# Optimization experiments

Measured on AMD Instinct MI355X. Metric: run time of the kernel, lower is better.

## Reference

```python
import jax, jax.numpy as jnp
import numpy as np

EPS = 1e-8


def setup_inputs() -> dict:
    key = jax.random.key(0)
    ks = jax.random.split(key, 5)
    B, C, F, T = 2, 8, 1024, 256
    Ch, Fh = 4 * C, 4 * F  # expanded channels/features
    s_pw1 = 1.0 / np.sqrt(F)
    s_dw1 = 1.0 / np.sqrt(C)
    s_pw2 = 1.0 / np.sqrt(Fh)
    s_dw2 = 1.0 / np.sqrt(Ch)
    return {
        "x": jax.random.normal(ks[0], (B, C, F, T), jnp.float32),
        "ln_w": jnp.ones((C, F), jnp.float32),
        "ln_b": jnp.zeros((C, F), jnp.float32),
        "pw1": jax.random.uniform(ks[1], (C, Fh, F), jnp.float32, -s_pw1, s_pw1),
        "dw1": jax.random.uniform(ks[2], (Ch, C), jnp.float32, -s_dw1, s_dw1),
        "pw2": jax.random.uniform(ks[3], (Ch, F, Fh), jnp.float32, -s_pw2, s_pw2),
        "dw2": jax.random.uniform(ks[4], (C, Ch), jnp.float32, -s_dw2, s_dw2),
    }


def _mc_layernorm(x, w, b):
    # x: (B,C,F,T); normalize over feature axis (2), affine per (channel, feature)
    mu = jnp.mean(x, axis=2, keepdims=True)
    var = jnp.var(x, axis=2, keepdims=True)
    xn = (x - mu) * jax.lax.rsqrt(var + EPS)
    return xn * w[None, :, :, None] + b[None, :, :, None]


def reference(x, ln_w, ln_b, pw1, dw1, pw2, dw2):
    h = _mc_layernorm(x, ln_w, ln_b)
    # per-channel positionwise linear: (C, F_out, F_in)
    h = jnp.einsum('bcft,cgf->bcgt', h, pw1)
    # channel mixing (depthwise linear across channels): (C_out, C_in)
    h = jnp.einsum('bcft,dc->bdft', h, dw1)
    h = jnp.square(jax.nn.relu(h))  # squared ReLU
    h = jnp.einsum('bcft,cgf->bcgt', h, pw2)
    h = jnp.einsum('bcft,dc->bdft', h, dw2)
    return x + h
```

## Files before the change

kernel.cpp:

```cpp
#include <hip/hip_runtime.h>

#define B_DIM  2
#define C_DIM  8
#define F_DIM  1024
#define T_DIM  256
#define CH_DIM 32
#define FH_DIM 4096
#define BT_DIM 512

typedef __bf16 bf16x8 __attribute__((ext_vector_type(8)));
typedef __bf16 bf16x4 __attribute__((ext_vector_type(4)));
typedef float  f32x4  __attribute__((ext_vector_type(4)));

__device__ __forceinline__ void async16(const void* g, void* l) {
  __builtin_amdgcn_global_load_lds(
      (const __attribute__((address_space(1))) unsigned int*)g,
      (__attribute__((address_space(3))) unsigned int*)l, 16, 0, 0);
}

#define LGKM0_SCHED() do { \
    asm volatile("s_waitcnt lgkmcnt(0)" ::: "memory"); \
    __builtin_amdgcn_sched_barrier(0); } while (0)

__global__ void ln_kernel(const float* __restrict__ x,
                          const float* __restrict__ lnw,
                          const float* __restrict__ lnb,
                          __bf16* __restrict__ hn) {
  const int tb = blockIdx.x;
  const int c  = blockIdx.y;
  const int b  = blockIdx.z;
  const int tid = threadIdx.x;
  const int t0 = tb * 16;

  extern __shared__ __align__(16) float xs[];
  __shared__ float ps[16][64], ps2[16][64];
  __shared__ float mean_s[16], rstd_s[16];

  const float* xp = x + (size_t)(b * C_DIM + c) * F_DIM * T_DIM;

  const int fbase = tid >> 2;
  const int tq    = tid & 3;

  float s0 = 0.f, s1 = 0.f, s2v = 0.f, s3 = 0.f;
  float q0 = 0.f, q1 = 0.f, q2 = 0.f, q3 = 0.f;
#pragma unroll 4
  for (int it = 0; it < 16; ++it) {
    const int f = it * 64 + fbase;
    const float4 v = *(const float4*)(xp + (size_t)f * T_DIM + t0 + tq * 4);
    xs[(tq * 4 + 0) * 1028 + f] = v.x;
    xs[(tq * 4 + 1) * 1028 + f] = v.y;
    xs[(tq * 4 + 2) * 1028 + f] = v.z;
    xs[(tq * 4 + 3) * 1028 + f] = v.w;
    s0 += v.x; q0 += v.x * v.x;
    s1 += v.y; q1 += v.y * v.y;
    s2v += v.z; q2 += v.z * v.z;
    s3 += v.w; q3 += v.w * v.w;
  }
  ps[tq * 4 + 0][fbase] = s0;  ps2[tq * 4 + 0][fbase] = q0;
  ps[tq * 4 + 1][fbase] = s1;  ps2[tq * 4 + 1][fbase] = q1;
  ps[tq * 4 + 2][fbase] = s2v; ps2[tq * 4 + 2][fbase] = q2;
  ps[tq * 4 + 3][fbase] = s3;  ps2[tq * 4 + 3][fbase] = q3;
  __syncthreads();
  if (tid < 16) {
    float a = 0.f, a2 = 0.f;
    for (int j = 0; j < 64; ++j) { a += ps[tid][j]; a2 += ps2[tid][j]; }
    const float mu  = a * (1.0f / F_DIM);
    const float var = a2 * (1.0f / F_DIM) - mu * mu;
    mean_s[tid] = mu;
    rstd_s[tid] = rsqrtf(var + 1e-8f);
  }
  __syncthreads();

  const int wv = tid >> 6, lane = tid & 63;
  const float* lw = lnw + c * F_DIM;
  const float* lb = lnb + c * F_DIM;
#pragma unroll
  for (int p = 0; p < 4; ++p) {
    const int t = wv * 4 + p;
    const float mu = mean_s[t], rs = rstd_s[t];
    __bf16* hp = hn + ((size_t)c * BT_DIM + b * T_DIM + t0 + t) * F_DIM;
#pragma unroll
    for (int j = 0; j < 8; ++j) {
      const int f = j * 128 + lane * 2;
      const float a = xs[t * 1028 + f];
      const float bb = xs[t * 1028 + f + 1];
      const float r0 = (a - mu) * rs * lw[f] + lb[f];
      const float r1 = (bb - mu) * rs * lw[f + 1] + lb[f + 1];
      __bf16 o2[2] = { (__bf16)r0, (__bf16)r1 };
      *(ushort*)nullptr == *(ushort*)nullptr;
      *(uint*)(hp + f) = *(uint*)o2;
    }
  }
}

template<int TPB_BITS, bool CT>
__global__ __launch_bounds__(512, 2)
void gemm_4p(const float* __restrict__ A, const __bf16* __restrict__ Bm,
             __bf16* __restrict__ Co, const int M, const int K) {
  const int NT = K >> 6;
  const int bid = blockIdx.x;
  const int xcd = bid & 7, idx = bid >> 3;
  const int batch = xcd * (32 >> TPB_BITS) + (idx >> TPB_BITS);
  const int tile  = idx & ((1 << TPB_BITS) - 1);
  const int mt = tile >> 1, nt = tile & 1;

  const int tid = threadIdx.x, lane = tid & 63, wid = tid >> 6;

  const float*  Ab = A  + (size_t)batch * M * K + (size_t)(mt * 256) * K;
  const __bf16* Bb = Bm + (size_t)batch * BT_DIM * K + (size_t)(nt * 256) * K;

  extern __shared__ __align__(16) char smem[];
  __bf16* const AS = (__bf16*)smem;
  __bf16* const BS = (__bf16*)(smem + 65536);

  const int wm = wid >> 2, wn = wid & 3;
  const int lr = lane & 15, khi = lane >> 4;
  const int lsw = lr & 7;

  const int b_row = lane >> 3;
  const int b_src = (lane & 7) ^ b_row;

  f32x4 acc[8][4] = {};
  float4 sa[8];
  bf16x8 af[4];

  auto issueB1 = [&](int sbuf, int tt, int j) {
    const int chunk = j * 8 + wid;
    async16(Bb + (size_t)(chunk * 8 + b_row) * K + (size_t)tt * 64 + b_src * 8,
            BS + sbuf * 16384 + chunk * 512);
  };
  auto issueA2 = [&](int tt, int i0) {
#pragma unroll
    for (int i = i0; i < i0 + 2; ++i) {
      const int c = i * 512 + tid;
      sa[i] = *(const float4*)(Ab + (size_t)(c >> 4) * K + (size_t)tt * 64 + (c & 15) * 4);
    }
  };
  auto writeA2 = [&](int abuf, int i0) {
#pragma unroll
    for (int i = i0; i < i0 + 2; ++i) {
      const int c = i * 512 + tid;
      const int r = c >> 4;
      const int s = ((c & 15) >> 1) ^ (r & 7);
      bf16x4 v;
      v[0]=(__bf16)sa[i].x; v[1]=(__bf16)sa[i].y; v[2]=(__bf16)sa[i].z; v[3]=(__bf16)sa[i].w;
      *(bf16x4*)(AS + abuf * 16384 + r * 64 + s * 8 + (c & 1) * 4) = v;
    }
  };
  auto readA = [&](int abuf, int mq, int ks) {
#pragma unroll
    for (int j = 0; j < 4; ++j) {
      const int row = wm * 128 + (mq * 4 + j) * 16 + lr;
      af[j] = *(const bf16x8*)(AS + abuf * 16384 + row * 64 + (((ks << 2) | khi) ^ lsw) * 8);
    }
  };
  auto readB4 = [&](bf16x8* bq, int rbuf, int ks) {
#pragma unroll
    for (int ni = 0; ni < 4; ++ni) {
      const int row = wn * 64 + ni * 16 + lr;
      bq[ni] = *(const bf16x8*)(BS + rbuf * 16384 + row * 64 + (((ks << 2) | khi) ^ lsw) * 8);
    }
  };
  auto mfma16 = [&](const bf16x8* bq, int mq) {
    __builtin_amdgcn_s_setprio(1);
#pragma unroll
    for (int j = 0; j < 4; ++j)
#pragma unroll
      for (int n = 0; n < 4; ++n)
        acc[mq * 4 + j][n] =
            __builtin_amdgcn_mfma_f32_16x16x32_bf16(af[j], bq[n], acc[mq * 4 + j][n], 0, 0, 0);
    __builtin_amdgcn_s_setprio(0);
  };

  issueA2(0, 0); issueA2(0, 2); issueA2(0, 4); issueA2(0, 6);
  issueB1(0, 0, 0); issueB1(0, 0, 1); issueB1(0, 0, 2); issueB1(0, 0, 3);
  issueB1(1, 1, 0); issueB1(1, 1, 1); issueB1(1, 1, 2); issueB1(1, 1, 3);
  writeA2(0, 0); writeA2(0, 2); writeA2(0, 4); writeA2(0, 6);
  issueA2(1, 0); issueA2(1, 2); issueA2(1, 4); issueA2(1, 6);
  asm volatile("s_waitcnt vmcnt(12)" ::: "memory");
  LGKM0_SCHED();
  __builtin_amdgcn_s_barrier();

  int cur = 0;
  for (int t = 0; t < NT; ++t) {
    const int rd = t % 3, st = (t + 2) % 3;
    const int tN = (t + 2 < NT) ? t + 2 : NT - 1;
    bf16x8 bq[4];
    issueB1(st, tN, 0); issueB1(st, tN, 1);
    readA(cur, 0, 0); readB4(bq, rd, 0);
    __builtin_amdgcn_s_barrier(); LGKM0_SCHED();
    mfma16(bq, 0); __builtin_amdgcn_s_barrier();
    issueB1(st, tN, 2); issueB1(st, tN, 3);
    readA(cur, 1, 0);
    __builtin_amdgcn_s_barrier(); LGKM0_SCHED();
    mfma16(bq, 1); __builtin_amdgcn_s_barrier();
    writeA2(cur ^ 1, 0); issueA2(tN, 0);
    writeA2(cur ^ 1, 2); issueA2(tN, 2);
    readA(cur, 0, 1); readB4(bq, rd, 1);
    __builtin_amdgcn_s_barrier(); LGKM0_SCHED();
    mfma16(bq, 0); __builtin_amdgcn_s_barrier();
    writeA2(cur ^ 1, 4); issueA2(tN, 4);
    writeA2(cur ^ 1, 6); issueA2(tN, 6);
    readA(cur, 1, 1);
    __builtin_amdgcn_s_barrier(); LGKM0_SCHED();
    mfma16(bq, 1);
    __builtin_amdgcn_s_barrier();
    cur ^= 1;
  }

  const int colc = lane & 15;
  const int rowb = (lane >> 4) * 4;
  if (CT) {
    __bf16* T = (__bf16*)smem + wid * 1152;
#pragma unroll
    for (int h = 0; h < 2; ++h) {
      const int mbase = mt * 256 + wm * 128 + h * 64;
#pragma unroll
      for (int ni = 0; ni < 4; ++ni) {
#pragma unroll
        for (int mi = 0; mi < 4; ++mi)
#pragma unroll
          for (int r = 0; r < 4; ++r)
            T[colc * 72 + mi * 16 + rowb + r] = (__bf16)acc[h * 4 + mi][ni][r];
        __bf16* outp = Co + (size_t)batch * BT_DIM * M
                          + (size_t)(nt * 256 + wn * 64 + ni * 16) * M + mbase + lane;
#pragma unroll
        for (int r16 = 0; r16 < 16; ++r16)
          outp[(size_t)r16 * M] = T[r16 * 72 + lane];
      }
    }
  } else {
#pragma unroll
    for (int mi = 0; mi < 8; ++mi) {
#pragma unroll
      for (int ni = 0; ni < 4; ++ni) {
        const int m = mt * 256 + wm * 128 + mi * 16 + rowb;
        const int n = nt * 256 + wn * 64 + ni * 16 + colc;
#pragma unroll
        for (int r = 0; r < 4; ++r)
          Co[((size_t)batch * M + m + r) * BT_DIM + n] = (__bf16)acc[mi][ni][r];
      }
    }
  }
}

__global__ void mix1_kernel(const __bf16* __restrict__ Y1,
                            const float* __restrict__ dw1,
                            __bf16* __restrict__ h2) {
  const int gidx = blockIdx.x * 256 + threadIdx.x;
  const int g8 = gidx & 511, bt = gidx >> 9;
  const int g0 = g8 * 8;

  float y[C_DIM][8];
#pragma unroll
  for (int c = 0; c < C_DIM; ++c) {
    bf16x8 v = *(const bf16x8*)(Y1 + ((size_t)c * BT_DIM + bt) * FH_DIM + g0);
#pragma unroll
    for (int j = 0; j < 8; ++j) y[c][j] = (float)v[j];
  }
  for (int d = 0; d < CH_DIM; ++d) {
    float s[8] = {0.f,0.f,0.f,0.f,0.f,0.f,0.f,0.f};
#pragma unroll
    for (int c = 0; c < C_DIM; ++c) {
      const float wv = dw1[d * C_DIM + c];
#pragma unroll
      for (int j = 0; j < 8; ++j) s[j] += wv * y[c][j];
    }
    bf16x8 o;
#pragma unroll
    for (int j = 0; j < 8; ++j) {
      float r = s[j] > 0.f ? s[j] : 0.f;
      o[j] = (__bf16)(r * r);
    }
    *(bf16x8*)(h2 + ((size_t)d * BT_DIM + bt) * FH_DIM + g0) = o;
  }
}

__global__ void mix2_kernel(const float* __restrict__ x,
                            const __bf16* __restrict__ Y2,
                            const float* __restrict__ dw2,
                            float* __restrict__ out) {
  const int gidx = blockIdx.x * 256 + threadIdx.x;
  const int t4 = gidx & 63;
  const int f  = (gidx >> 6) & 1023;
  const int b  = gidx >> 16;
  const int t0 = t4 * 4;

  float4 r[C_DIM];
#pragma unroll
  for (int dd = 0; dd < C_DIM; ++dd)
    r[dd] = *(const float4*)(x + ((size_t)(b * C_DIM + dd) * F_DIM + f) * T_DIM + t0);

  for (int d = 0; d < CH_DIM; ++d) {
    bf16x4 v = *(const bf16x4*)(Y2 + ((size_t)d * F_DIM + f) * BT_DIM + b * T_DIM + t0);
    const float v0 = (float)v[0], v1 = (float)v[1], v2 = (float)v[2], v3 = (float)v[3];
#pragma unroll
    for (int dd = 0; dd < C_DIM; ++dd) {
      const float w = dw2[dd * CH_DIM + d];
      r[dd].x += w * v0; r[dd].y += w * v1; r[dd].z += w * v2; r[dd].w += w * v3;
    }
  }
#pragma unroll
  for (int dd = 0; dd < C_DIM; ++dd)
    *(float4*)(out + ((size_t)(b * C_DIM + dd) * F_DIM + f) * T_DIM + t0) = r[dd];
}

extern "C" void kernel_launch(void* const* d_in, const int* in_sizes, int n_in,
                              void* d_out, int out_size, void* d_ws, size_t ws_size,
                              hipStream_t stream) {
  const float* x   = (const float*)d_in[0];
  const float* lnw = (const float*)d_in[1];
  const float* lnb = (const float*)d_in[2];
  const float* pw1 = (const float*)d_in[3];
  const float* dw1 = (const float*)d_in[4];
  const float* pw2 = (const float*)d_in[5];
  const float* dw2 = (const float*)d_in[6];
  float* out = (float*)d_out;

  char* ws = (char*)d_ws;
  __bf16* hn = (__bf16*)(ws);
  __bf16* Y1 = (__bf16*)(ws + (8ULL << 20));
  __bf16* h2 = (__bf16*)(ws + (40ULL << 20));
  __bf16* Y2 = (__bf16*)(ws);

  (void)hipFuncSetAttribute((const void*)ln_kernel,
                            hipFuncAttributeMaxDynamicSharedMemorySize, 65792);
  (void)hipFuncSetAttribute((const void*)gemm_4p<5, true>,
                            hipFuncAttributeMaxDynamicSharedMemorySize, 163840);
  (void)hipFuncSetAttribute((const void*)gemm_4p<3, false>,
                            hipFuncAttributeMaxDynamicSharedMemorySize, 163840);

  ln_kernel<<<dim3(T_DIM / 16, C_DIM, B_DIM), 256, 65792, stream>>>(x, lnw, lnb, hn);
  gemm_4p<5, true><<<256, 512, 163840, stream>>>(pw1, hn, Y1, FH_DIM, F_DIM);
  mix1_kernel<<<(BT_DIM * (FH_DIM / 8)) / 256, 256, 0, stream>>>(Y1, dw1, h2);
  gemm_4p<3, false><<<256, 512, 163840, stream>>>(pw2, h2, Y2, F_DIM, FH_DIM);
  mix2_kernel<<<512, 256, 0, stream>>>(x, Y2, dw2, out);
}
```

Before: 293.7 us.

## Replace pw2 GEMM with smaller-tile double-buffered kernel using more blocks

Replaces the second per-channel GEMM (pw2 over K=4096) with a dedicated kernel that uses 128x128 tiles, 256 threads, static double-buffered LDS and register-staged fp32-to-bf16 conversion of A. It launches 1024 blocks instead of 256 so more CUs get work and several blocks can be resident per CU. The cost is smaller tiles, which means less reuse per loaded byte and more A traffic. It also removes a stray null-pointer comparison statement in the layernorm kernel.

```diff
diff --git a/kernel.cpp b/kernel.cpp
--- a/kernel.cpp
+++ b/kernel.cpp
@@ -87,7 +87,6 @@
       const float r0 = (a - mu) * rs * lw[f] + lb[f];
       const float r1 = (bb - mu) * rs * lw[f + 1] + lb[f + 1];
       __bf16 o2[2] = { (__bf16)r0, (__bf16)r1 };
-      *(ushort*)nullptr == *(ushort*)nullptr;
       *(uint*)(hp + f) = *(uint*)o2;
     }
   }
@@ -244,6 +243,111 @@
   }
 }
 
+__global__ __launch_bounds__(256, 3)
+void gemm_pw2(const float* __restrict__ A, const __bf16* __restrict__ Bm,
+              __bf16* __restrict__ Co) {
+  const int M = F_DIM, K = FH_DIM;
+  const int bid = blockIdx.x;
+  const int xcd = bid & 7, idx = bid >> 3;
+  const int q   = idx & 31;
+  const int nt  = idx >> 5;
+  const int batch = xcd * 4 + (q >> 3);
+  const int mt    = q & 7;
+
+  const int tid = threadIdx.x, lane = tid & 63, wid = tid >> 6;
+
+  const float*  Ab = A  + (size_t)batch * M * K + (size_t)(mt * 128) * K;
+  const __bf16* Bb = Bm + (size_t)batch * BT_DIM * K + (size_t)(nt * 128) * K;
+
+  __shared__ __align__(16) __bf16 As[2][128 * 32];
+  __shared__ __align__(16) __bf16 Bs[2][128 * 32];
+
+  const int a_r  = tid >> 3;
+  const int a_c8 = tid & 7;
+
+  const int wm = (wid >> 1) * 64, wn = (wid & 1) * 64;
+  const int lr = lane & 15, khi = lane >> 4;
+  const int lswz = (lr >> 1) & 3;
+
+  f32x4 acc[4][4] = {};
+  float4 sa[4];
+  const int NT = K >> 5;
+
+  auto issueA = [&](int tt) {
+#pragma unroll
+    for (int i = 0; i < 4; ++i)
+      sa[i] = *(const float4*)(Ab + (size_t)(a_r + 32 * i) * K + tt * 32 + a_c8 * 4);
+  };
+  auto writeA = [&](int buf) {
+#pragma unroll
+    for (int i = 0; i < 4; ++i) {
+      const int row = a_r + 32 * i;
+      bf16x4 v;
+      v[0] = (__bf16)sa[i].x; v[1] = (__bf16)sa[i].y;
+      v[2] = (__bf16)sa[i].z; v[3] = (__bf16)sa[i].w;
+      const int slot = (a_c8 >> 1) ^ ((row >> 1) & 3);
+      *(bf16x4*)(&As[buf][row * 32 + slot * 8 + (a_c8 & 1) * 4]) = v;
+    }
+  };
+  auto issueB = [&](int buf, int tt) {
+#pragma unroll
+    for (int j = 0; j < 2; ++j) {
+      const int chunk = wid * 2 + j;
+      const int r = chunk * 16 + (lane >> 2);
+      const int s = (lane & 3) ^ ((r >> 1) & 3);
+      async16(Bb + (size_t)r * K + (size_t)tt * 32 + s * 8,
+              &Bs[buf][chunk * 512]);
+    }
+  };
+  auto compute = [&](int buf) {
+    bf16x8 af[4], bq[4];
+    const int soff = (khi ^ lswz) * 8;
+#pragma unroll
+    for (int mi = 0; mi < 4; ++mi)
+      af[mi] = *(const bf16x8*)(&As[buf][(wm + mi * 16 + lr) * 32 + soff]);
+#pragma unroll
+    for (int ni = 0; ni < 4; ++ni)
+      bq[ni] = *(const bf16x8*)(&Bs[buf][(wn + ni * 16 + lr) * 32 + soff]);
+    __builtin_amdgcn_s_setprio(1);
+#pragma unroll
+    for (int mi = 0; mi < 4; ++mi)
+#pragma unroll
+      for (int ni = 0; ni < 4; ++ni)
+        acc[mi][ni] = __builtin_amdgcn_mfma_f32_16x16x32_bf16(af[mi], bq[ni], acc[mi][ni], 0, 0, 0);
+    __builtin_amdgcn_s_setprio(0);
+  };
+
+  issueA(0);
+  issueB(0, 0);
+  writeA(0);
+  __syncthreads();
+
+  int buf = 0;
+  for (int t = 0; t < NT; ++t) {
+    const int tn = (t + 1 < NT) ? t + 1 : t;
+    issueA(tn);
+    issueB(buf ^ 1, tn);
+    compute(buf);
+    writeA(buf ^ 1);
+    __syncthreads();
+    buf ^= 1;
+  }
+
+  const int colc = lane & 15;
+  const int rowb = (lane >> 4) * 4;
+#pragma unroll
+  for (int mi = 0; mi < 4; ++mi) {
+#pragma unroll
+    for (int ni = 0; ni < 4; ++ni) {
+      const int m = mt * 128 + wm + mi * 16 + rowb;
+      const int n = nt * 128 + wn + ni * 16 + colc;
+#pragma unroll
+      for (int r = 0; r < 4; ++r)
+        Co[((size_t)batch * M + m + r) * BT_DIM + n] = (__bf16)acc[mi][ni][r];
+    }
+  }
+}
+
 __global__ void mix1_kernel(const __bf16* __restrict__ Y1,
                             const float* __restrict__ dw1,
                             __bf16* __restrict__ h2) {
@@ -327,12 +431,10 @@
                             hipFuncAttributeMaxDynamicSharedMemorySize, 65792);
   (void)hipFuncSetAttribute((const void*)gemm_4p<5, true>,
                             hipFuncAttributeMaxDynamicSharedMemorySize, 163840);
-  (void)hipFuncSetAttribute((const void*)gemm_4p<3, false>,
-                            hipFuncAttributeMaxDynamicSharedMemorySize, 163840);
 
   ln_kernel<<<dim3(T_DIM / 16, C_DIM, B_DIM), 256, 65792, stream>>>(x, lnw, lnb, hn);
   gemm_4p<5, true><<<256, 512, 163840, stream>>>(pw1, hn, Y1, FH_DIM, F_DIM);
   mix1_kernel<<<(BT_DIM * (FH_DIM / 8)) / 256, 256, 0, stream>>>(Y1, dw1, h2);
-  gemm_4p<3, false><<<256, 512, 163840, stream>>>(pw2, h2, Y2, F_DIM, FH_DIM);
+  gemm_pw2<<<1024, 256, 0, stream>>>(pw2, h2, Y2);
   mix2_kernel<<<512, 256, 0, stream>>>(x, Y2, dw2, out);
 }
```

New measurement: 537.1 us. +82.9%, slower.
